# Kernel tuning notes

Measured on AMD Instinct MI355X. Metric: run time of the kernel, lower is better.

## Reference

```python
import jax, jax.numpy as jnp
import numpy as np

B, S, H, V = 2, 2048, 1024, 32000
SDS = [64, 128, 256]
EPS = 1e-5


def _ln(x, g, b):
    m = jnp.mean(x, -1, keepdims=True)
    v = jnp.var(x, -1, keepdims=True)
    return (x - m) * jax.lax.rsqrt(v + EPS) * g + b


def _layer(x, A_log, Wb, Wc, D, Wg, bg, Wo, bo, g, be):
    # x: [B,S,H]; state dim N = A_log.shape[0]
    A = jnp.exp(A_log)
    gate = jax.nn.sigmoid(jnp.einsum('bsh,nh->bsn', x, Wg) + bg)
    Bx = jnp.einsum('bsh,nh->bsn', x, Wb)
    u = gate * Bx  # [B,S,N]

    def step(s, u_t):
        s = A * s + u_t
        return s, s

    s0 = jnp.zeros((x.shape[0], A.shape[0]), x.dtype)
    _, states = jax.lax.scan(step, s0, jnp.swapaxes(u, 0, 1))  # [S,B,N]
    states = jnp.swapaxes(states, 0, 1)
    y = jnp.einsum('bsn,hn->bsh', states, Wc) + D * x
    out = _ln(y + x, g, be)
    return out @ Wo.T + bo  # dropout is identity (p used in eval / p=0)


def setup_inputs() -> dict:
    key = jax.random.key(0)
    ks = iter(jax.random.split(key, 64))
    d = {}
    d['x'] = jax.random.randint(next(ks), (B, S), 0, V)
    d['E'] = jax.random.normal(next(ks), (V, H), jnp.float32) * 0.02
    for i, N in enumerate(SDS):
        d[f'A{i}'] = jnp.log(jnp.exp(jnp.full((N,), -0.5)) + 0.1 * jax.random.normal(next(ks), (N,)))
        d[f'Wb{i}'] = jax.random.normal(next(ks), (N, H), jnp.float32) * 0.02
        d[f'Wc{i}'] = jax.random.normal(next(ks), (H, N), jnp.float32) * 0.02
        d[f'D{i}'] = jax.random.normal(next(ks), (H,), jnp.float32)
        d[f'Wg{i}'] = jax.random.normal(next(ks), (N, H), jnp.float32) * 0.02
        d[f'bg{i}'] = jnp.zeros((N,), jnp.float32)
        d[f'Wo{i}'] = jax.random.normal(next(ks), (H, H), jnp.float32) * 0.02
        d[f'bo{i}'] = jnp.zeros((H,), jnp.float32)
        d[f'g{i}'] = jnp.ones((H,), jnp.float32)
        d[f'be{i}'] = jnp.zeros((H,), jnp.float32)
    d['Wf'] = jax.random.normal(next(ks), (H, 3 * H), jnp.float32) * 0.02
    d['bf'] = jnp.zeros((H,), jnp.float32)
    d['gf'] = jnp.ones((H,), jnp.float32)
    d['bef'] = jnp.zeros((H,), jnp.float32)
    d['Wh'] = jax.random.normal(next(ks), (V, H), jnp.float32) * 0.02
    d['bh'] = jnp.zeros((V,), jnp.float32)
    return d


def reference(x, E,
              A0, Wb0, Wc0, D0, Wg0, bg0, Wo0, bo0, g0, be0,
              A1, Wb1, Wc1, D1, Wg1, bg1, Wo1, bo1, g1, be1,
              A2, Wb2, Wc2, D2, Wg2, bg2, Wo2, bo2, g2, be2,
              Wf, bf, gf, bef, Wh, bh):
    emb = E[x]  # [B,S,H]
    o0 = _layer(emb, A0, Wb0, Wc0, D0, Wg0, bg0, Wo0, bo0, g0, be0)
    o1 = _layer(emb, A1, Wb1, Wc1, D1, Wg1, bg1, Wo1, bo1, g1, be1)
    o2 = _layer(emb, A2, Wb2, Wc2, D2, Wg2, bg2, Wo2, bo2, g2, be2)
    combined = jnp.concatenate([o0, o1, o2], axis=-1)  # [B,S,3H]
    fused = combined @ Wf.T + bf
    fused = _ln(fused + emb, gf, bef)
    logits = fused @ Wh.T + bh  # [B,S,V]
    return logits
```

## Files before the change

### kernel.cpp

```cpp
#include <hip/hip_runtime.h>
#include <hip/hip_bf16.h>

#define Hd 1024
#define Bdim 2
#define Sd 2048
#define BSd 4096
#define Vd 32000
#define EPSf 1e-5f
#define CH 16
#define NCH 128
#define NT3 448

typedef __attribute__((ext_vector_type(8))) short short8;
typedef __attribute__((ext_vector_type(4))) float f32x4;
typedef __attribute__((ext_vector_type(4))) unsigned short us4;

__device__ __forceinline__ unsigned short f2bf(float f) {
  union { float f; unsigned int u; } v; v.f = f;
  return (unsigned short)((v.u + 0x7fffu + ((v.u >> 16) & 1u)) >> 16);
}

typedef __attribute__((address_space(1))) const void gvoid_t;
typedef __attribute__((address_space(3))) void svoid_t;
__device__ __forceinline__ void gl_lds16(const void* g, void* s) {
  __builtin_amdgcn_global_load_lds((gvoid_t*)g, (svoid_t*)s, 16, 0, 0);
}

struct CvtTab {
  const float* src[11];
  unsigned short* dst[11];
  int start[12];
};
__global__ void k_cvt_all(CvtTab tab) {
  int b = blockIdx.x;
  int j = 0;
  while (j < 10 && b >= tab.start[j + 1]) ++j;
  size_t i = (size_t)(b - tab.start[j]) * 256 + threadIdx.x;
  f32x4 v = *(const f32x4*)(tab.src[j] + i * 4);
  us4 o;
  o[0] = f2bf(v[0]); o[1] = f2bf(v[1]); o[2] = f2bf(v[2]); o[3] = f2bf(v[3]);
  *(us4*)(tab.dst[j] + i * 4) = o;
}

__global__ void k_cvtT(const float* __restrict__ s0, const float* __restrict__ s1,
                       const float* __restrict__ s2, unsigned short* __restrict__ dst) {
  const float* src = blockIdx.z == 0 ? s0 : (blockIdx.z == 1 ? s1 : s2);
  unsigned short* d = dst + (size_t)blockIdx.z * Hd * Hd;
  __shared__ float tile[32][33];
  int tx = threadIdx.x & 31, ty = threadIdx.x >> 5;
  int bx = blockIdx.x * 32, by = blockIdx.y * 32;
  #pragma unroll
  for (int i = 0; i < 4; ++i)
    tile[ty + i * 8][tx] = src[(size_t)(by + ty + i * 8) * Hd + bx + tx];
  __syncthreads();
  #pragma unroll
  for (int i = 0; i < 4; ++i)
    d[(size_t)(bx + ty + i * 8) * Hd + by + tx] = f2bf(tile[tx][ty + i * 8]);
}

__global__ void k_biasf(const float* __restrict__ Wf_, const float* __restrict__ bfb,
                        const float* __restrict__ bo0, const float* __restrict__ bo1,
                        const float* __restrict__ bo2, float* __restrict__ biasf) {
  int h = blockIdx.x, t = threadIdx.x;
  float s = 0.f;
  for (int c = t; c < 3072; c += 256) {
    float b = c < 1024 ? bo0[c] : (c < 2048 ? bo1[c - 1024] : bo2[c - 2048]);
    s += Wf_[(size_t)h * 3072 + c] * b;
  }
  #pragma unroll
  for (int o = 32; o >= 1; o >>= 1) s += __shfl_xor(s, o);
  __shared__ float red[4];
  if ((t & 63) == 0) red[t >> 6] = s;
  __syncthreads();
  if (t == 0) biasf[h] = bfb[h] + red[0] + red[1] + red[2] + red[3];
}

__global__ void k_setup(const float* A0, const float* A1, const float* A2,
                        const float* b0, const float* b1, const float* b2,
                        const float* D0, const float* D1, const float* D2,
                        const float* g0, const float* g1, const float* g2,
                        const float* e0, const float* e1, const float* e2,
                        float* Alog448, float* bg448,
                        float* D3, float* g3, float* be3) {
  int t = blockIdx.x * 256 + threadIdx.x;
  if (t < NT3) {
    int l = t < 64 ? 0 : (t < 192 ? 1 : 2);
    int o = t - (l == 0 ? 0 : (l == 1 ? 64 : 192));
    Alog448[t] = (l == 0 ? A0 : (l == 1 ? A1 : A2))[o];
    bg448[t]   = (l == 0 ? b0 : (l == 1 ? b1 : b2))[o];
  }
  if (t < 3072) {
    int l = t >> 10, o = t & 1023;
    D3[t]  = (l == 0 ? D0 : (l == 1 ? D1 : D2))[o];
    g3[t]  = (l == 0 ? g0 : (l == 1 ? g1 : g2))[o];
    be3[t] = (l == 0 ? e0 : (l == 1 ? e1 : e2))[o];
  }
}

__global__ void k_embed(const int* __restrict__ x, const float* __restrict__ E,
                        float* __restrict__ emb, unsigned short* __restrict__ embbf) {
  int row = blockIdx.x, t = threadIdx.x;
  int id = x[row];
  f32x4 v = *(const f32x4*)(E + (size_t)id * Hd + t * 4);
  *(f32x4*)(emb + (size_t)row * Hd + t * 4) = v;
  us4 o;
  o[0] = f2bf(v[0]); o[1] = f2bf(v[1]); o[2] = f2bf(v[2]); o[3] = f2bf(v[3]);
  *(us4*)(embbf + (size_t)row * Hd + t * 4) = o;
}

template<int BM, int BN, int WM, int WN, int BF16_OUT>
__launch_bounds__(WM * WN * 64)
__global__ void gemm2ph(const unsigned short* __restrict__ A,
                        const unsigned short* __restrict__ Bw,
                        const float* __restrict__ bias,
                        void* __restrict__ Cv,
                        int N, int K, int lda, int ldb, int ldc, int coff, int tm)
{
  constexpr int NT = WM * WN * 64;
  constexpr int MF = BM / WM / 16;
  constexpr int NF = BN / WN / 16;
  constexpr int ASZ = BM * 64;
  constexpr int BSZ = BN * 64;
  constexpr int AR = (ASZ * 2) / (NT * 16);
  constexpr int BR = (BSZ * 2) / (NT * 16);
  __shared__ __align__(16) unsigned short Sm[2 * (ASZ + BSZ)];

  int T = gridDim.x;
  int orig = blockIdx.x;
  int q = T >> 3, r = T & 7;
  int xc = orig & 7, sdv = orig >> 3;
  int wgid = (xc < r ? xc * (q + 1) : r * (q + 1) + (xc - r) * q) + sdv;
  int n_t = wgid / tm, m_t = wgid % tm;
  int row0 = m_t * BM, col0 = n_t * BN;

  int tid = threadIdx.x;
  int wave = tid >> 6, lane = tid & 63;
  int wm = wave / WN, wn = wave % WN;
  int wr = wm * (BM / WM), wc = wn * (BN / WN);
  int lr = lane & 15;
  int klane = lane >> 4;

  f32x4 acc[MF][NF] = {};

  auto stage = [&](int buf, int k0) {
    unsigned short* Ab = Sm + buf * (ASZ + BSZ);
    unsigned short* Bb = Ab + ASZ;
    #pragma unroll
    for (int j = 0; j < AR; ++j) {
      int slot = j * NT + tid;
      int lrow = slot >> 3, c16 = slot & 7;
      int scol = (c16 ^ (lrow & 7)) * 8;
      gl_lds16(A + (size_t)(row0 + lrow) * lda + k0 + scol, Ab + (j * NT + wave * 64) * 8);
    }
    #pragma unroll
    for (int j = 0; j < BR; ++j) {
      int slot = j * NT + tid;
      int lrow = slot >> 3, c16 = slot & 7;
      int scol = (c16 ^ (lrow & 7)) * 8;
      int brow = col0 + lrow;
      if (brow >= N) brow = N - 1;
      gl_lds16(Bw + (size_t)brow * ldb + k0 + scol, Bb + (j * NT + wave * 64) * 8);
    }
  };

  auto compute = [&](int buf) {
    const unsigned short* Ab = Sm + buf * (ASZ + BSZ);
    const unsigned short* Bb = Ab + ASZ;
    #pragma unroll
    for (int kk = 0; kk < 2; ++kk) {
      short8 afr[MF], bfr[NF];
      #pragma unroll
      for (int m = 0; m < MF; ++m) {
        int row = wr + m * 16 + lr;
        int cs = (kk * 4 + klane) ^ (row & 7);
        afr[m] = *(const short8*)(Ab + row * 64 + cs * 8);
      }
      #pragma unroll
      for (int n = 0; n < NF; ++n) {
        int row = wc + n * 16 + lr;
        int cs = (kk * 4 + klane) ^ (row & 7);
        bfr[n] = *(const short8*)(Bb + row * 64 + cs * 8);
      }
      #pragma unroll
      for (int m = 0; m < MF; ++m)
        #pragma unroll
        for (int n = 0; n < NF; ++n)
          acc[m][n] = __builtin_amdgcn_mfma_f32_16x16x32_bf16(afr[m], bfr[n], acc[m][n], 0, 0, 0);
    }
  };

  int nt = K >> 6;
  stage(0, 0);
  __syncthreads();
  for (int t = 0; t < nt - 1; ++t) {
    stage((t & 1) ^ 1, (t + 1) * 64);
    compute(t & 1);
    __syncthreads();
  }
  compute((nt - 1) & 1);

  int rb = (lane >> 4) * 4;
  #pragma unroll
  for (int m = 0; m < MF; ++m) {
    #pragma unroll
    for (int n = 0; n < NF; ++n) {
      int gcol = col0 + wc + n * 16 + lr;
      if (gcol >= N) continue;
      float bv = bias ? bias[gcol] : 0.f;
      #pragma unroll
      for (int j = 0; j < 4; ++j) {
        int grow = row0 + wr + m * 16 + rb + j;
        float val = acc[m][n][j] + bv;
        if (BF16_OUT)
          ((unsigned short*)Cv)[(size_t)grow * ldc + coff + gcol] = f2bf(val);
        else
          ((float*)Cv)[(size_t)grow * ldc + coff + gcol] = val;
      }
    }
  }
}

__launch_bounds__(512)
__global__ void gemm8ph(const unsigned short* __restrict__ A,
                        const unsigned short* __restrict__ Bw,
                        const float* __restrict__ bias,
                        float* __restrict__ Cv,
                        int N, int K, int lda, int ldb, int ldc, int tm)
{
  __shared__ __align__(16) unsigned short Sm[65536];

  int T = gridDim.x;
  int orig = blockIdx.x;
  int q = T >> 3, r = T & 7;
  int xc = orig & 7, sdv = orig >> 3;
  int wgid = (xc < r ? xc * (q + 1) : r * (q + 1) + (xc - r) * q) + sdv;
  int n_t = wgid / tm, m_t = wgid % tm;
  int row0 = m_t * 256, col0 = n_t * 256;

  int tid = threadIdx.x;
  int wave = tid >> 6, lane = tid & 63;
  int wm = wave >> 2, wn = wave & 3;
  int lr = lane & 15, klane = lane >> 4;

  f32x4 acc[8][4] = {};

  auto stageA = [&](int b, int h, int kt) {
    unsigned short* base = Sm + (b * 2 + h) * 8192;
    #pragma unroll
    for (int j = 0; j < 2; ++j) {
      int slot = j * 512 + tid;
      int lrow = slot >> 3, c16 = slot & 7;
      int scol = (c16 ^ (lrow & 7)) * 8;
      gl_lds16(A + (size_t)(row0 + h * 128 + lrow) * lda + kt * 64 + scol,
               base + (j * 512 + wave * 64) * 8);
    }
  };
  auto stageB = [&](int b, int h, int kt) {
    unsigned short* base = Sm + 32768 + (b * 2 + h) * 8192;
    #pragma unroll
    for (int j = 0; j < 2; ++j) {
      int slot = j * 512 + tid;
      int lrow = slot >> 3, c16 = slot & 7;
      int scol = (c16 ^ (lrow & 7)) * 8;
      gl_lds16(Bw + (size_t)(col0 + h * 128 + lrow) * ldb + kt * 64 + scol,
               base + (j * 512 + wave * 64) * 8);
    }
  };
  auto readA = [&](short8* afr, int b, int mh, int kk) {
    const unsigned short* base = Sm + (b * 2 + mh) * 8192;
    #pragma unroll
    for (int f = 0; f < 4; ++f) {
      int rowin = f * 32 + wm * 16 + lr;
      int cs = (kk * 4 + klane) ^ (rowin & 7);
      afr[f] = *(const short8*)(base + rowin * 64 + cs * 8);
    }
  };
  auto readB = [&](short8* bfr, int b, int kk) {
    #pragma unroll
    for (int n = 0; n < 4; ++n) {
      int rowin = (n & 1) * 64 + wn * 16 + lr;
      const unsigned short* base = Sm + 32768 + (b * 2 + (n >> 1)) * 8192;
      int cs = (kk * 4 + klane) ^ (rowin & 7);
      bfr[n] = *(const short8*)(base + rowin * 64 + cs * 8);
    }
  };

  #define MFMA16(mh, afr, bfr)                                                  \
    __builtin_amdgcn_s_setprio(1);                                              \
    _Pragma("unroll")                                                           \
    for (int f = 0; f < 4; ++f)                                                 \
      _Pragma("unroll")                                                         \
      for (int n = 0; n < 4; ++n)                                               \
        acc[(mh) * 4 + f][n] = __builtin_amdgcn_mfma_f32_16x16x32_bf16(         \
            afr[f], bfr[n], acc[(mh) * 4 + f][n], 0, 0, 0);                     \
    __builtin_amdgcn_s_setprio(0);

  #define BAR()   __builtin_amdgcn_s_barrier()
  #define FEN()   asm volatile("" ::: "memory")
  #define VM4()   asm volatile("s_waitcnt vmcnt(4)" ::: "memory")
  #define VM0()   asm volatile("s_waitcnt vmcnt(0)" ::: "memory")

  int nt = K >> 6;
  int iters = K >> 7;

  stageA(0, 0, 0); stageB(0, 0, 0); stageB(0, 1, 0); stageA(0, 1, 0);
  stageA(1, 0, 1); stageB(1, 0, 1);
  VM4(); BAR();

  short8 afr[4], bfr0[4], bfr1[4];
  for (int i = 0; i < iters; ++i) {
    int t1 = 2 * i + 1, t2 = 2 * i + 2, t3 = 2 * i + 3;
    bool last = (i == iters - 1);
    readA(afr, 0, 0, 0); readB(bfr0, 0, 0);
    BAR(); FEN();
    stageB(1, 1, t1); stageA(1, 1, t1);
    MFMA16(0, afr, bfr0);
    BAR();
    readA(afr, 0, 0, 1); readB(bfr1, 0, 1);
    BAR(); FEN();
    MFMA16(0, afr, bfr1);
    BAR();
    readA(afr, 0, 1, 0);
    BAR(); FEN();
    if (t2 < nt) stageA(0, 0, t2);
    MFMA16(1, afr, bfr0);
    BAR();
    readA(afr, 0, 1, 1);
    BAR(); FEN();
    if (t2 < nt) stageB(0, 0, t2);
    MFMA16(1, afr, bfr1);
    if (last) { VM0(); } else { VM4(); }
    BAR();
    readA(afr, 1, 0, 0); readB(bfr0, 1, 0);
    BAR(); FEN();
    if (t2 < nt) { stageB(0, 1, t2); stageA(0, 1, t2); }
    MFMA16(0, afr, bfr0);
    BAR();
    readA(afr, 1, 0, 1); readB(bfr1, 1, 1);
    BAR(); FEN();
    MFMA16(0, afr, bfr1);
    BAR();
    readA(afr, 1, 1, 0);
    BAR(); FEN();
    if (t3 < nt) stageA(1, 0, t3);
    MFMA16(1, afr, bfr0);
    BAR();
    readA(afr, 1, 1, 1);
    BAR(); FEN();
    if (t3 < nt) stageB(1, 0, t3);
    MFMA16(1, afr, bfr1);
    if (!last) { VM4(); }
    BAR();
  }

  int rb = (lane >> 4) * 4;
  #pragma unroll
  for (int idx = 0; idx < 8; ++idx) {
    int mh = idx >> 2, f = idx & 3;
    int growb = row0 + mh * 128 + f * 32 + wm * 16 + rb;
    #pragma unroll
    for (int n = 0; n < 4; ++n) {
      int gcol = col0 + (n & 1) * 64 + (n >> 1) * 128 + wn * 16 + lr;
      float bv = bias[gcol];
      #pragma unroll
      for (int j = 0; j < 4; ++j)
        Cv[(size_t)(growb + j) * ldc + gcol] = acc[idx][n][j] + bv;
    }
  }
  #undef MFMA16
  #undef BAR
  #undef FEN
  #undef VM4
  #undef VM0
}

__global__ void k_scanA(const float* __restrict__ gzbx, const float* __restrict__ Alog448,
                        const float* __restrict__ bg448,
                        float* __restrict__ st, float* __restrict__ carry) {
  int gid = blockIdx.x * 256 + threadIdx.x;
  if (gid >= Bdim * NCH * NT3) return;
  int n = gid % NT3;
  int c = (gid / NT3) % NCH;
  int b = gid / (NT3 * NCH);
  float a = expf(Alog448[n]);
  float bgv = bg448[n];
  float s = 0.f;
  size_t rbase = (size_t)b * Sd + (size_t)c * CH;
  for (int t = 0; t < CH; ++t) {
    size_t row = rbase + t;
    float gzv = gzbx[row * 896 + n];
    float bxv = gzbx[row * 896 + 448 + n];
    float gv = 1.f / (1.f + expf(-(gzv + bgv)));
    s = a * s + gv * bxv;
    st[row * NT3 + n] = s;
  }
  carry[((size_t)b * NCH + c) * NT3 + n] = s;
}

__global__ void k_scanB(const float* __restrict__ carry, const float* __restrict__ Alog448,
                        float* __restrict__ cin) {
  int i = blockIdx.x * 256 + threadIdx.x;
  if (i >= Bdim * NT3) return;
  int b = i / NT3, n = i % NT3;
  float aC = expf((float)CH * Alog448[n]);
  float s = 0.f;
  for (int c = 0; c < NCH; ++c) {
    cin[((size_t)b * NCH + c) * NT3 + n] = s;
    s = aC * s + carry[((size_t)b * NCH + c) * NT3 + n];
  }
}

__global__ void k_scanC(const float* __restrict__ st, const float* __restrict__ cin,
                        const float* __restrict__ Alog448, unsigned short* __restrict__ stbf) {
  size_t gid = (size_t)blockIdx.x * 256 + threadIdx.x;
  if (gid >= (size_t)BSd * NT3) return;
  int n = gid % NT3;
  int row = gid / NT3;
  int b = row / Sd, sg = row % Sd;
  int c = sg / CH, t = sg % CH;
  float cv = cin[((size_t)b * NCH + c) * NT3 + n];
  float val = st[gid] + expf((float)(t + 1) * Alog448[n]) * cv;
  stbf[gid] = f2bf(val);
}

__global__ void k_ln3(const float* __restrict__ y3, const float* __restrict__ emb,
                      const float* __restrict__ D3, const float* __restrict__ g3,
                      const float* __restrict__ be3, unsigned short* __restrict__ z3) {
  int row = blockIdx.x, ly = blockIdx.y, t = threadIdx.x;
  const float* y = y3 + (size_t)row * 3072 + ly * 1024;
  f32x4 yv = *(const f32x4*)(y + t * 4);
  f32x4 ev = *(const f32x4*)(emb + (size_t)row * Hd + t * 4);
  float vals[4];
  float sum = 0.f, sq = 0.f;
  #pragma unroll
  for (int j = 0; j < 4; ++j) {
    float coef = D3[ly * 1024 + t * 4 + j] + 1.f;
    float v = yv[j] + coef * ev[j];
    vals[j] = v; sum += v; sq += v * v;
  }
  #pragma unroll
  for (int o = 32; o >= 1; o >>= 1) {
    sum += __shfl_xor(sum, o);
    sq += __shfl_xor(sq, o);
  }
  __shared__ float red[2][4];
  int w = t >> 6, lane = t & 63;
  if (lane == 0) { red[0][w] = sum; red[1][w] = sq; }
  __syncthreads();
  sum = red[0][0] + red[0][1] + red[0][2] + red[0][3];
  sq  = red[1][0] + red[1][1] + red[1][2] + red[1][3];
  float mean = sum * (1.f / Hd);
  float var = sq * (1.f / Hd) - mean * mean;
  float rs = rsqrtf(var + EPSf);
  us4 o4;
  #pragma unroll
  for (int j = 0; j < 4; ++j) {
    float z = (vals[j] - mean) * rs * g3[ly * 1024 + t * 4 + j] + be3[ly * 1024 + t * 4 + j];
    o4[j] = f2bf(z);
  }
  *(us4*)(z3 + (size_t)row * 3072 + ly * 1024 + t * 4) = o4;
}

__global__ void k_ln(const float* __restrict__ y, const float* __restrict__ emb,
                     const float* __restrict__ g, const float* __restrict__ be,
                     unsigned short* __restrict__ out) {
  int row = blockIdx.x, t = threadIdx.x;
  f32x4 yv = *(const f32x4*)(y + (size_t)row * Hd + t * 4);
  f32x4 ev = *(const f32x4*)(emb + (size_t)row * Hd + t * 4);
  float vals[4];
  float sum = 0.f, sq = 0.f;
  #pragma unroll
  for (int j = 0; j < 4; ++j) {
    float v = yv[j] + ev[j];
    vals[j] = v; sum += v; sq += v * v;
  }
  #pragma unroll
  for (int o = 32; o >= 1; o >>= 1) {
    sum += __shfl_xor(sum, o);
    sq += __shfl_xor(sq, o);
  }
  __shared__ float red[2][4];
  int w = t >> 6, lane = t & 63;
  if (lane == 0) { red[0][w] = sum; red[1][w] = sq; }
  __syncthreads();
  sum = red[0][0] + red[0][1] + red[0][2] + red[0][3];
  sq  = red[1][0] + red[1][1] + red[1][2] + red[1][3];
  float mean = sum * (1.f / Hd);
  float var = sq * (1.f / Hd) - mean * mean;
  float rs = rsqrtf(var + EPSf);
  us4 o4;
  #pragma unroll
  for (int j = 0; j < 4; ++j) {
    float z = (vals[j] - mean) * rs * g[t * 4 + j] + be[t * 4 + j];
    o4[j] = f2bf(z);
  }
  *(us4*)(out + (size_t)row * Hd + t * 4) = o4;
}

extern "C" void kernel_launch(void* const* d_in, const int* in_sizes, int n_in,
                              void* d_out, int out_size, void* d_ws, size_t ws_size,
                              hipStream_t stream) {
  (void)in_sizes; (void)n_in; (void)out_size; (void)ws_size;
  const int* x = (const int*)d_in[0];
  const float* E = (const float*)d_in[1];
  const float* Wf_ = (const float*)d_in[32];
  const float* bfb = (const float*)d_in[33];
  const float* gfp = (const float*)d_in[34];
  const float* bef = (const float*)d_in[35];
  const float* Wh_ = (const float*)d_in[36];
  const float* bh = (const float*)d_in[37];

  char* wsb = (char*)d_ws;
  size_t off = 0;
  auto alloc = [&](size_t bytes) -> void* {
    void* p = wsb + off;
    off += (bytes + 255) & ~(size_t)255;
    return p;
  };
  float* emb             = (float*)alloc((size_t)BSd * Hd * 4);
  unsigned short* embbf  = (unsigned short*)alloc((size_t)BSd * Hd * 2);
  unsigned short* wgwbbf = (unsigned short*)alloc((size_t)896 * Hd * 2);
  unsigned short* wcbf   = (unsigned short*)alloc((size_t)NT3 * Hd * 2);
  unsigned short* wotbf  = (unsigned short*)alloc((size_t)3 * Hd * Hd * 2);
  unsigned short* wfbf   = (unsigned short*)alloc((size_t)3 * Hd * Hd * 2);
  unsigned short* wcombbf= (unsigned short*)alloc((size_t)Hd * 3 * Hd * 2);
  unsigned short* whbf   = (unsigned short*)alloc((size_t)Vd * Hd * 2);
  float* gzbx            = (float*)alloc((size_t)BSd * 896 * 4);
  float* stl             = (float*)alloc((size_t)BSd * NT3 * 4);
  unsigned short* stbf   = (unsigned short*)alloc((size_t)BSd * NT3 * 2);
  float* carry           = (float*)alloc((size_t)Bdim * NCH * NT3 * 4);
  float* cin             = (float*)alloc((size_t)Bdim * NCH * NT3 * 4);
  float* ybuf3           = (float*)alloc((size_t)BSd * 3072 * 4);
  unsigned short* zbf3   = (unsigned short*)alloc((size_t)BSd * 3072 * 2);
  unsigned short* zbf    = (unsigned short*)alloc((size_t)BSd * Hd * 2);
  float* Alog448         = (float*)alloc(NT3 * 4);
  float* bg448           = (float*)alloc(NT3 * 4);
  float* D3              = (float*)alloc(3072 * 4);
  float* g3              = (float*)alloc(3072 * 4);
  float* be3             = (float*)alloc(3072 * 4);
  float* biasf           = (float*)alloc(Hd * 4);

  k_embed<<<BSd, 256, 0, stream>>>(x, E, emb, embbf);

  {
    CvtTab tab;
    const int rowoff_g[3] = {0, 64, 192};
    int j = 0;
    int n4s[11];
    for (int i = 0; i < 3; ++i) { tab.src[j] = (const float*)d_in[2 + 10 * i + 4]; tab.dst[j] = wgwbbf + (size_t)rowoff_g[i] * Hd;         n4s[j] = (64 << i) * Hd / 4; ++j; }
    for (int i = 0; i < 3; ++i) { tab.src[j] = (const float*)d_in[2 + 10 * i + 1]; tab.dst[j] = wgwbbf + (size_t)(448 + rowoff_g[i]) * Hd;  n4s[j] = (64 << i) * Hd / 4; ++j; }
    for (int i = 0; i < 3; ++i) { tab.src[j] = (const float*)d_in[2 + 10 * i + 2]; tab.dst[j] = wcbf + (size_t)rowoff_g[i] * Hd;            n4s[j] = (64 << i) * Hd / 4; ++j; }
    tab.src[j] = Wf_; tab.dst[j] = wfbf; n4s[j] = 3 * Hd * Hd / 4; ++j;
    tab.src[j] = Wh_; tab.dst[j] = whbf; n4s[j] = Vd * Hd / 4; ++j;
    tab.start[0] = 0;
    for (int k = 0; k < 11; ++k) tab.start[k + 1] = tab.start[k] + (n4s[k] + 255) / 256;
    k_cvt_all<<<tab.start[11], 256, 0, stream>>>(tab);
  }

  k_cvtT<<<dim3(32, 32, 3), 256, 0, stream>>>(
      (const float*)d_in[8], (const float*)d_in[18], (const float*)d_in[28], wotbf);

  k_setup<<<12, 256, 0, stream>>>(
      (const float*)d_in[2], (const float*)d_in[12], (const float*)d_in[22],
      (const float*)d_in[7], (const float*)d_in[17], (const float*)d_in[27],
      (const float*)d_in[5], (const float*)d_in[15], (const float*)d_in[25],
      (const float*)d_in[10], (const float*)d_in[20], (const float*)d_in[30],
      (const float*)d_in[11], (const float*)d_in[21], (const float*)d_in[31],
      Alog448, bg448, D3, g3, be3);

  k_biasf<<<Hd, 256, 0, stream>>>(Wf_, bfb,
      (const float*)d_in[9], (const float*)d_in[19], (const float*)d_in[29], biasf);

  for (int i = 0; i < 3; ++i) {
    gemm2ph<128,128,2,2,1><<<(Hd / 128) * (Hd / 128), 256, 0, stream>>>(
        wfbf + i * Hd, wotbf + (size_t)i * Hd * Hd, nullptr, wcombbf,
        Hd, Hd, 3 * Hd, Hd, 3 * Hd, i * Hd, Hd / 128);
  }

  const int TM = BSd / 128;

  gemm2ph<128,128,2,2,0><<<(896 / 128) * TM, 256, 0, stream>>>(
      embbf, wgwbbf, nullptr, gzbx, 896, Hd, Hd, Hd, 896, 0, TM);

  {
    int totA = Bdim * NCH * NT3;
    k_scanA<<<(totA + 255) / 256, 256, 0, stream>>>(gzbx, Alog448, bg448, stl, carry);
    k_scanB<<<(Bdim * NT3 + 255) / 256, 256, 0, stream>>>(carry, Alog448, cin);
    size_t totC = (size_t)BSd * NT3;
    k_scanC<<<(int)((totC + 255) / 256), 256, 0, stream>>>(stl, cin, Alog448, stbf);
  }

  const int owg[3] = {0, 64, 192};
  const int sd[3] = {64, 128, 256};
  for (int i = 0; i < 3; ++i) {
    gemm2ph<128,128,2,2,0><<<(Hd / 128) * TM, 256, 0, stream>>>(
        stbf + owg[i], wcbf + (size_t)owg[i] * Hd, nullptr, ybuf3,
        Hd, sd[i], NT3, sd[i], 3072, i * Hd, TM);
  }

  k_ln3<<<dim3(BSd, 3), 256, 0, stream>>>(ybuf3, emb, D3, g3, be3, zbf3);

  gemm2ph<128,128,2,2,0><<<(Hd / 128) * TM, 256, 0, stream>>>(
      zbf3, wcombbf, biasf, ybuf3, Hd, 3 * Hd, 3 * Hd, 3 * Hd, Hd, 0, TM);
  k_ln<<<BSd, 256, 0, stream>>>(ybuf3, emb, gfp, bef, zbf);

  const int TM256 = BSd / 256;
  gemm8ph<<<(Vd / 256) * TM256, 512, 0, stream>>>(
      zbf, whbf, bh, (float*)d_out, Vd, Hd, Hd, Hd, Vd, TM256);
}
```

Baseline: 620.3 us.

## Batch three weight-combine GEMMs into one launch and vectorize gemm8ph stores

The three per-layer Wf·Wo weight-combination GEMMs are replaced by a single batched kernel, gemm_bd3, launched with 192 workgroups. It uses a simple double-buffered LDS pipeline and writes bf16 output. In gemm8ph (the big logits GEMM) the MFMA operands are swapped so each lane holds four consecutive columns of a row. The epilogue can then issue 16-byte float4 stores with a vector bias load instead of strided scalar stores. The aim is fewer launches and better-coalesced output writes for the large [4096x32000] fp32 result; the swapped layout has to stay exactly consistent for correctness.

```diff
diff --git a/kernel.cpp b/kernel.cpp
--- a/kernel.cpp
+++ b/kernel.cpp
@@ -220,6 +220,91 @@
   }
 }
 
+__launch_bounds__(256)
+__global__ void gemm_bd3(const unsigned short* __restrict__ Awf,
+                         const unsigned short* __restrict__ Bwo,
+                         unsigned short* __restrict__ Cw)
+{
+  constexpr int ASZ = 128 * 64, BSZ = 128 * 64;
+  __shared__ __align__(16) unsigned short Sm[2 * (ASZ + BSZ)];
+  int T = gridDim.x;
+  int orig = blockIdx.x;
+  int q = T >> 3, r = T & 7;
+  int xc = orig & 7, sdv = orig >> 3;
+  int wgid = (xc < r ? xc * (q + 1) : r * (q + 1) + (xc - r) * q) + sdv;
+  int n_g = wgid / 8, m_t = wgid % 8;
+  int li = n_g >> 3, n_t = n_g & 7;
+  const unsigned short* A = Awf + li * Hd;
+  const unsigned short* Bw = Bwo + ((size_t)li << 20);
+  int row0 = m_t * 128, col0 = n_t * 128;
+
+  int tid = threadIdx.x;
+  int wave = tid >> 6, lane = tid & 63;
+  int wm = wave >> 1, wn = wave & 1;
+  int wr = wm * 64, wc = wn * 64;
+  int lr = lane & 15, klane = lane >> 4;
+
+  f32x4 acc[4][4] = {};
+  auto stage = [&](int buf, int k0) {
+    unsigned short* Ab = Sm + buf * (ASZ + BSZ);
+    unsigned short* Bb = Ab + ASZ;
+    #pragma unroll
+    for (int j = 0; j < 4; ++j) {
+      int slot = j * 256 + tid;
+      int lrow = slot >> 3, c16 = slot & 7;
+      int scol = (c16 ^ (lrow & 7)) * 8;
+      gl_lds16(A + (size_t)(row0 + lrow) * 3072 + k0 + scol, Ab + (j * 256 + wave * 64) * 8);
+      gl_lds16(Bw + (size_t)(col0 + lrow) * 1024 + k0 + scol, Bb + (j * 256 + wave * 64) * 8);
+    }
+  };
+  auto compute = [&](int buf) {
+    const unsigned short* Ab = Sm + buf * (ASZ + BSZ);
+    const unsigned short* Bb = Ab + ASZ;
+    #pragma unroll
+    for (int kk = 0; kk < 2; ++kk) {
+      short8 afr[4], bfr[4];
+      #pragma unroll
+      for (int m = 0; m < 4; ++m) {
+        int row = wr + m * 16 + lr;
+        int cs = (kk * 4 + klane) ^ (row & 7);
+        afr[m] = *(const short8*)(Ab + row * 64 + cs * 8);
+      }
+      #pragma unroll
+      for (int n = 0; n < 4; ++n) {
+        int row = wc + n * 16 + lr;
+        int cs = (kk * 4 + klane) ^ (row & 7);
+        bfr[n] = *(const short8*)(Bb + row * 64 + cs * 8);
+      }
+      #pragma unroll
+      for (int m = 0; m < 4; ++m)
+        #pragma unroll
+        for (int n = 0; n < 4; ++n)
+          acc[m][n] = __builtin_amdgcn_mfma_f32_16x16x32_bf16(afr[m], bfr[n], acc[m][n], 0, 0, 0);
+    }
+  };
+  stage(0, 0);
+  __syncthreads();
+  for (int t = 0; t < 15; ++t) {
+    stage((t & 1) ^ 1, (t + 1) * 64);
+    compute(t & 1);
+    __syncthreads();
+  }
+  compute(1);
+
+  int rb = (lane >> 4) * 4;
+  #pragma unroll
+  for (int m = 0; m < 4; ++m)
+    #pragma unroll
+    for (int n = 0; n < 4; ++n) {
+      int gcol = li * Hd + col0 + wc + n * 16 + lr;
+      #pragma unroll
+      for (int j = 0; j < 4; ++j) {
+        int grow = row0 + wr + m * 16 + rb + j;
+        Cw[(size_t)grow * 3072 + gcol] = f2bf(acc[m][n][j]);
+      }
+    }
+}
+
 __launch_bounds__(512)
 __global__ void gemm8ph(const unsigned short* __restrict__ A,
                         const unsigned short* __restrict__ Bw,
@@ -292,7 +377,7 @@
       _Pragma("unroll")                                                         \
       for (int n = 0; n < 4; ++n)                                               \
         acc[(mh) * 4 + f][n] = __builtin_amdgcn_mfma_f32_16x16x32_bf16(         \
-            afr[f], bfr[n], acc[(mh) * 4 + f][n], 0, 0, 0);                     \
+            bfr[n], afr[f], acc[(mh) * 4 + f][n], 0, 0, 0);                     \
     __builtin_amdgcn_s_setprio(0);
 
   #define BAR()   __builtin_amdgcn_s_barrier()
@@ -353,18 +438,22 @@
     BAR();
   }
 
-  int rb = (lane >> 4) * 4;
+  int cb = klane * 4;
   #pragma unroll
   for (int idx = 0; idx < 8; ++idx) {
     int mh = idx >> 2, f = idx & 3;
-    int growb = row0 + mh * 128 + f * 32 + wm * 16 + rb;
+    int grow = row0 + mh * 128 + f * 32 + wm * 16 + lr;
+    float* crow = Cv + (size_t)grow * ldc;
     #pragma unroll
     for (int n = 0; n < 4; ++n) {
-      int gcol = col0 + (n & 1) * 64 + (n >> 1) * 128 + wn * 16 + lr;
-      float bv = bias[gcol];
-      #pragma unroll
-      for (int j = 0; j < 4; ++j)
-        Cv[(size_t)(growb + j) * ldc + gcol] = acc[idx][n][j] + bv;
+      int gcol = col0 + (n & 1) * 64 + (n >> 1) * 128 + wn * 16 + cb;
+      f32x4 bv = *(const f32x4*)(bias + gcol);
+      f32x4 o;
+      o[0] = acc[idx][n][0] + bv[0];
+      o[1] = acc[idx][n][1] + bv[1];
+      o[2] = acc[idx][n][2] + bv[2];
+      o[3] = acc[idx][n][3] + bv[3];
+      *(f32x4*)(crow + gcol) = o;
     }
   }
   #undef MFMA16
@@ -571,11 +660,7 @@
   k_biasf<<<Hd, 256, 0, stream>>>(Wf_, bfb,
       (const float*)d_in[9], (const float*)d_in[19], (const float*)d_in[29], biasf);
 
-  for (int i = 0; i < 3; ++i) {
-    gemm2ph<128,128,2,2,1><<<(Hd / 128) * (Hd / 128), 256, 0, stream>>>(
-        wfbf + i * Hd, wotbf + (size_t)i * Hd * Hd, nullptr, wcombbf,
-        Hd, Hd, 3 * Hd, Hd, 3 * Hd, i * Hd, Hd / 128);
-  }
+  gemm_bd3<<<192, 256, 0, stream>>>(wfbf, wotbf, wcombbf);
 
   const int TM = BSd / 128;
 
```

Result: no change. 616.7 us (-0.6%).
